# Kernel tuning notes

Measured on AMD Instinct MI355X. Metric: run time of the kernel, lower is better.

Reference implementation:

```python
import jax, jax.numpy as jnp
import numpy as np

D_MODEL = 1024
NUM_HEADS = 16
DEPTH = D_MODEL // NUM_HEADS


def setup_inputs() -> dict:
    key = jax.random.key(0)
    ks = jax.random.split(key, 9)
    B, S = 2, 2048
    s = 1.0 / np.sqrt(D_MODEL)
    return {
        "x": jax.random.normal(ks[0], (B, S, D_MODEL), dtype=jnp.float32),
        "wq": jax.random.normal(ks[1], (D_MODEL, D_MODEL), dtype=jnp.float32) * s,
        "bq": jnp.zeros((D_MODEL,), dtype=jnp.float32),
        "wk": jax.random.normal(ks[2], (D_MODEL, D_MODEL), dtype=jnp.float32) * s,
        "bk": jnp.zeros((D_MODEL,), dtype=jnp.float32),
        "wv": jax.random.normal(ks[3], (D_MODEL, D_MODEL), dtype=jnp.float32) * s,
        "bv": jnp.zeros((D_MODEL,), dtype=jnp.float32),
        "wo": jax.random.normal(ks[4], (D_MODEL, D_MODEL), dtype=jnp.float32) * s,
        "bo": jnp.zeros((D_MODEL,), dtype=jnp.float32),
    }


def _split_heads(t):
    # [B, S, D] -> [B, H, S, depth]
    B, S, _ = t.shape
    return t.reshape(B, S, NUM_HEADS, DEPTH).transpose(0, 2, 1, 3)


def reference(x, wq, bq, wk, bk, wv, bv, wo, bo):
    B, S, _ = x.shape
    q = _split_heads(x @ wq + bq)
    k = _split_heads(x @ wk + bk)
    v = _split_heads(x @ wv + bv)
    scale = 1.0 / jnp.sqrt(jnp.asarray(DEPTH, dtype=x.dtype))
    logits = jnp.einsum("bhsd,bhtd->bhst", q, k) * scale  # [B,H,S,S]
    attn = jax.nn.softmax(logits, axis=-1)
    ctx = jnp.einsum("bhst,bhtd->bhsd", attn, v)  # [B,H,S,depth]
    concat = ctx.transpose(0, 2, 1, 3).reshape(B, S, D_MODEL)
    return concat @ wo + bo
```

## Files before the change

kernel.cpp:

```cpp
#include <hip/hip_runtime.h>
#include <hip/hip_bf16.h>

typedef __bf16 bf16;
typedef __bf16 bf16x4 __attribute__((ext_vector_type(4)));
typedef __bf16 bf16x8 __attribute__((ext_vector_type(8)));
typedef float f32x4 __attribute__((ext_vector_type(4)));

typedef __attribute__((address_space(3))) void lds_void;
typedef const __attribute__((address_space(1))) void gbl_void;

#define D_MODEL 1024
#define NHEAD 16
#define DEPTH 64
#define SEQ 2048
#define BATCH 2
#define NTOK (BATCH * SEQ)

#define Q_SCALE 0.18033688f

__global__ __launch_bounds__(256) void prep(const float* __restrict__ w0,
                                            const float* __restrict__ w1,
                                            const float* __restrict__ w2,
                                            const float* __restrict__ w3,
                                            const float* __restrict__ x,
                                            bf16* __restrict__ wtb,
                                            bf16* __restrict__ xb) {
    int z = blockIdx.z;
    int tx = threadIdx.x, ty = threadIdx.y;
    if (z < 4) {
        const float* w = (z == 0) ? w0 : (z == 1) ? w1 : (z == 2) ? w2 : w3;
        bf16* d = wtb + (size_t)z * D_MODEL * D_MODEL;
        __shared__ float tile[32][33];
        int c0 = blockIdx.x * 32;
        int r0 = blockIdx.y * 32;
#pragma unroll
        for (int i = 0; i < 4; i++)
            tile[ty + i * 8][tx] = w[(size_t)(r0 + ty + i * 8) * D_MODEL + c0 + tx];
        __syncthreads();
#pragma unroll
        for (int i = 0; i < 4; i++)
            d[(size_t)(c0 + ty + i * 8) * D_MODEL + r0 + tx] = (bf16)tile[tx][ty + i * 8];
    } else {
        int t = ty * 32 + tx;
        size_t i = ((size_t)(z - 4) * 1024 + blockIdx.y * 32 + blockIdx.x) * 256 + t;
        float4 v = ((const float4*)x)[i];
        bf16x4 o = {(bf16)v.x, (bf16)v.y, (bf16)v.z, (bf16)v.w};
        *(bf16x4*)&xb[i * 4] = o;
    }
}

template <bool SWAP>
__device__ __forceinline__ void gemm_core(const bf16* __restrict__ A,
                                          const bf16* __restrict__ Bt,
                                          int row0, int col0,
                                          bf16* As, bf16* Bs, f32x4 acc[4][4]) {
    const int tid = threadIdx.x;
    const int lane = tid & 63, wave = tid >> 6;
    const int quad = lane >> 4, l16 = lane & 15;
    const int wm = (wave & 1) << 6, wn = (wave >> 1) << 6;
    const int srow = lane >> 2, selem = (lane & 3) * 8;

    for (int k0 = 0; k0 < D_MODEL; k0 += 32) {
        __syncthreads();
#pragma unroll
        for (int t = 0; t < 2; t++) {
            int m = wave * 2 + t;
            const bf16* ga = A + (size_t)(row0 + m * 16 + srow) * D_MODEL + k0 + selem;
            const bf16* gb = Bt + (size_t)(col0 + m * 16 + srow) * D_MODEL + k0 + selem;
            __builtin_amdgcn_global_load_lds((gbl_void*)ga, (lds_void*)(As + m * 512 + lane * 8), 16, 0, 0);
            __builtin_amdgcn_global_load_lds((gbl_void*)gb, (lds_void*)(Bs + m * 512 + lane * 8), 16, 0, 0);
        }
        __syncthreads();
        bf16x8 af[4], bfr[4];
#pragma unroll
        for (int i = 0; i < 4; i++)
            af[i] = *(const bf16x8*)&As[(wm + i * 16 + l16) * 32 + quad * 8];
#pragma unroll
        for (int j = 0; j < 4; j++)
            bfr[j] = *(const bf16x8*)&Bs[(wn + j * 16 + l16) * 32 + quad * 8];
#pragma unroll
        for (int i = 0; i < 4; i++)
#pragma unroll
            for (int j = 0; j < 4; j++)
                acc[i][j] = SWAP
                    ? __builtin_amdgcn_mfma_f32_16x16x32_bf16(bfr[j], af[i], acc[i][j], 0, 0, 0)
                    : __builtin_amdgcn_mfma_f32_16x16x32_bf16(af[i], bfr[j], acc[i][j], 0, 0, 0);
    }
}

__global__ __launch_bounds__(256) void qkv_gemm(const bf16* __restrict__ xb,
                                                const bf16* __restrict__ wtb,
                                                const float* __restrict__ bq,
                                                const float* __restrict__ bk,
                                                const float* __restrict__ bv,
                                                bf16* __restrict__ q,
                                                bf16* __restrict__ k,
                                                bf16* __restrict__ v) {
    __shared__ bf16 As[128 * 32];
    __shared__ bf16 Bs[128 * 32];
    int zc = blockIdx.x;
    int z = zc >> 3;
    const bf16* Bt = wtb + (size_t)z * D_MODEL * D_MODEL;
    const float* bias = (z == 0) ? bq : (z == 1) ? bk : bv;
    int row0 = blockIdx.y * 128, col0 = (zc & 7) * 128;
    f32x4 acc[4][4] = {};

    const int lane = threadIdx.x & 63, wave = threadIdx.x >> 6;
    const int quad = lane >> 4, l16 = lane & 15;
    const int wm = (wave & 1) << 6, wn = (wave >> 1) << 6;

    if (z < 2) {
        gemm_core<false>(xb, Bt, row0, col0, As, Bs, acc);
        bf16* dst = (z == 0) ? q : k;
        const float sc = (z == 0) ? Q_SCALE : 1.0f;
#pragma unroll
        for (int i = 0; i < 4; i++) {
#pragma unroll
            for (int j = 0; j < 4; j++) {
                int colg = col0 + wn + j * 16 + l16;
                int hh = colg >> 6, d = colg & 63;
                float bi = bias[colg];
                int rbase = row0 + wm + i * 16 + quad * 4;
                int b = rbase >> 11, sb = rbase & 2047;
#pragma unroll
                for (int r = 0; r < 4; r++) {
                    size_t idx = ((size_t)(b * NHEAD + hh) * SEQ + sb + r) * DEPTH + d;
                    dst[idx] = (bf16)((acc[i][j][r] + bi) * sc);
                }
            }
        }
    } else {
        gemm_core<true>(xb, Bt, row0, col0, As, Bs, acc);
#pragma unroll
        for (int i = 0; i < 4; i++) {
            int tok = row0 + wm + i * 16 + l16;
            int b = tok >> 11, sb = tok & 2047;
#pragma unroll
            for (int j = 0; j < 4; j++) {
#pragma unroll
                for (int r = 0; r < 4; r++) {
                    int f = col0 + wn + j * 16 + quad * 4 + r;
                    int hh = f >> 6, d = f & 63;
                    v[((size_t)(b * NHEAD + hh) * DEPTH + d) * SEQ + sb] =
                        (bf16)(acc[i][j][r] + bias[f]);
                }
            }
        }
    }
}

__global__ __launch_bounds__(256) void attn(const bf16* __restrict__ q,
                                            const bf16* __restrict__ k,
                                            const bf16* __restrict__ v,
                                            bf16* __restrict__ ctx) {
    __shared__ bf16 Ks[64 * 72];
    __shared__ bf16 Vs[64 * 72];
    __shared__ bf16 Ps[4][32 * 72];
    const int tid = threadIdx.x;
    const int lane = tid & 63, wave = tid >> 6;
    const int quad = lane >> 4, l16 = lane & 15;
    const int bh = blockIdx.x;
    const int q0 = blockIdx.y * 128;
    const size_t hb = (size_t)bh * SEQ * DEPTH;
    const bf16* qh = q + hb;
    const bf16* kh = k + hb;
    const bf16* vh = v + hb;

    bf16x8 bq_[2][2];
#pragma unroll
    for (int g = 0; g < 2; g++) {
        int qrow = q0 + wave * 32 + g * 16 + l16;
#pragma unroll
        for (int c = 0; c < 2; c++)
            bq_[g][c] = *(const bf16x8*)&qh[(size_t)qrow * DEPTH + c * 32 + quad * 8];
    }
    bf16* myP = &Ps[wave][0];

    bf16x8 ones;
#pragma unroll
    for (int i = 0; i < 8; i++) ones[i] = (bf16)1.0f;

    f32x4 ov[2][4] = {};
    f32x4 lacc[2] = {};

    const int srow = tid >> 2, scol = (tid & 3) << 4;
    const bf16* kg = kh + (size_t)srow * DEPTH + scol;
    const bf16* vg = vh + (size_t)srow * SEQ + scol;
    bf16* ksd = &Ks[srow * 72 + scol];
    bf16* vsd = &Vs[srow * 72 + scol];

    bf16x8 kr0 = *(const bf16x8*)kg, kr1 = *(const bf16x8*)(kg + 8);
    bf16x8 vr0 = *(const bf16x8*)vg, vr1 = *(const bf16x8*)(vg + 8);

    for (int t0 = 0; t0 < SEQ; t0 += 64) {
        __syncthreads();
        *(bf16x8*)ksd = kr0;  *(bf16x8*)(ksd + 8) = kr1;
        *(bf16x8*)vsd = vr0;  *(bf16x8*)(vsd + 8) = vr1;
        __syncthreads();
        if (t0 + 64 < SEQ) {
            const bf16* kgn = kg + (size_t)(t0 + 64) * DEPTH;
            const bf16* vgn = vg + (t0 + 64);
            kr0 = *(const bf16x8*)kgn;  kr1 = *(const bf16x8*)(kgn + 8);
            vr0 = *(const bf16x8*)vgn;  vr1 = *(const bf16x8*)(vgn + 8);
        }
        f32x4 sc[2][4] = {};
#pragma unroll
        for (int c = 0; c < 2; c++)
#pragma unroll
            for (int j = 0; j < 4; j++) {
                bf16x8 kf = *(const bf16x8*)&Ks[(j * 16 + l16) * 72 + c * 32 + quad * 8];
#pragma unroll
                for (int g = 0; g < 2; g++)
                    sc[g][j] = __builtin_amdgcn_mfma_f32_16x16x32_bf16(kf, bq_[g][c], sc[g][j], 0, 0, 0);
            }
#pragma unroll
        for (int g = 0; g < 2; g++)
#pragma unroll
            for (int j = 0; j < 4; j++) {
                bf16x4 pb = {(bf16)__builtin_amdgcn_exp2f(sc[g][j][0]),
                             (bf16)__builtin_amdgcn_exp2f(sc[g][j][1]),
                             (bf16)__builtin_amdgcn_exp2f(sc[g][j][2]),
                             (bf16)__builtin_amdgcn_exp2f(sc[g][j][3])};
                *(bf16x4*)&myP[(g * 16 + l16) * 72 + j * 16 + quad * 4] = pb;
            }
#pragma unroll
        for (int c = 0; c < 2; c++) {
            bf16x8 pf[2];
#pragma unroll
            for (int g = 0; g < 2; g++) {
                pf[g] = *(const bf16x8*)&myP[(g * 16 + l16) * 72 + c * 32 + quad * 8];
                lacc[g] = __builtin_amdgcn_mfma_f32_16x16x32_bf16(ones, pf[g], lacc[g], 0, 0, 0);
            }
#pragma unroll
            for (int t = 0; t < 4; t++) {
                bf16x8 vf = *(const bf16x8*)&Vs[(t * 16 + l16) * 72 + c * 32 + quad * 8];
#pragma unroll
                for (int g = 0; g < 2; g++)
                    ov[g][t] = __builtin_amdgcn_mfma_f32_16x16x32_bf16(vf, pf[g], ov[g][t], 0, 0, 0);
            }
        }
    }
    int b = bh >> 4, hh = bh & 15;
#pragma unroll
    for (int g = 0; g < 2; g++) {
        float inv = 1.0f / lacc[g][0];
        size_t rowb = ((size_t)(b * SEQ + q0 + wave * 32 + g * 16 + l16)) * D_MODEL + hh * 64;
#pragma unroll
        for (int t = 0; t < 4; t++) {
            bf16x4 ob = {(bf16)(ov[g][t][0] * inv), (bf16)(ov[g][t][1] * inv),
                         (bf16)(ov[g][t][2] * inv), (bf16)(ov[g][t][3] * inv)};
            *(bf16x4*)&ctx[rowb + t * 16 + quad * 4] = ob;
        }
    }
}

__global__ __launch_bounds__(256) void out_gemm(const bf16* __restrict__ ctx,
                                                const bf16* __restrict__ wot,
                                                const float* __restrict__ bo,
                                                float* __restrict__ out) {
    __shared__ bf16 As[64 * 32];
    __shared__ bf16 Bs[128 * 32];
    const int tid = threadIdx.x;
    const int lane = tid & 63, wave = tid >> 6;
    const int quad = lane >> 4, l16 = lane & 15;
    const int srow = lane >> 2, selem = (lane & 3) * 8;
    int row0 = blockIdx.y * 64, col0 = blockIdx.x * 128;
    f32x4 acc[4][2] = {};

    for (int k0 = 0; k0 < D_MODEL; k0 += 32) {
        __syncthreads();
        {
            const bf16* ga = ctx + (size_t)(row0 + wave * 16 + srow) * D_MODEL + k0 + selem;
            __builtin_amdgcn_global_load_lds((gbl_void*)ga, (lds_void*)(As + wave * 512 + lane * 8), 16, 0, 0);
        }
#pragma unroll
        for (int t = 0; t < 2; t++) {
            int m = wave * 2 + t;
            const bf16* gb = wot + (size_t)(col0 + m * 16 + srow) * D_MODEL + k0 + selem;
            __builtin_amdgcn_global_load_lds((gbl_void*)gb, (lds_void*)(Bs + m * 512 + lane * 8), 16, 0, 0);
        }
        __syncthreads();
        bf16x8 af[4], bfr[2];
#pragma unroll
        for (int i = 0; i < 4; i++)
            af[i] = *(const bf16x8*)&As[(i * 16 + l16) * 32 + quad * 8];
#pragma unroll
        for (int j = 0; j < 2; j++)
            bfr[j] = *(const bf16x8*)&Bs[(wave * 32 + j * 16 + l16) * 32 + quad * 8];
#pragma unroll
        for (int i = 0; i < 4; i++)
#pragma unroll
            for (int j = 0; j < 2; j++)
                acc[i][j] = __builtin_amdgcn_mfma_f32_16x16x32_bf16(af[i], bfr[j], acc[i][j], 0, 0, 0);
    }
#pragma unroll
    for (int i = 0; i < 4; i++)
#pragma unroll
        for (int j = 0; j < 2; j++) {
            int colg = col0 + wave * 32 + j * 16 + l16;
            float bi = bo[colg];
            int rbase = row0 + i * 16 + quad * 4;
#pragma unroll
            for (int r = 0; r < 4; r++)
                out[(size_t)(rbase + r) * D_MODEL + colg] = acc[i][j][r] + bi;
        }
}

extern "C" void kernel_launch(void* const* d_in, const int* in_sizes, int n_in,
                              void* d_out, int out_size, void* d_ws, size_t ws_size,
                              hipStream_t stream) {
    const float* x  = (const float*)d_in[0];
    const float* wq = (const float*)d_in[1];
    const float* bq = (const float*)d_in[2];
    const float* wk = (const float*)d_in[3];
    const float* bk = (const float*)d_in[4];
    const float* wv = (const float*)d_in[5];
    const float* bv = (const float*)d_in[6];
    const float* wo = (const float*)d_in[7];
    const float* bo = (const float*)d_in[8];
    float* out = (float*)d_out;

    const size_t MB = 1024 * 1024;
    char* ws = (char*)d_ws;
    bf16* xb  = (bf16*)(ws);
    bf16* wtb = (bf16*)(ws + 8 * MB);
    bf16* qb  = (bf16*)(ws + 16 * MB);
    bf16* kb  = (bf16*)(ws + 24 * MB);
    bf16* vb  = (bf16*)(ws + 32 * MB);
    bf16* ctx = (bf16*)(ws + 40 * MB);

    prep<<<dim3(32, 32, 8), dim3(32, 8), 0, stream>>>(wq, wk, wv, wo, x, wtb, xb);
    qkv_gemm<<<dim3(24, 32), 256, 0, stream>>>(xb, wtb, bq, bk, bv, qb, kb, vb);
    attn<<<dim3(BATCH * NHEAD, SEQ / 128), 256, 0, stream>>>(qb, kb, vb, ctx);
    out_gemm<<<dim3(8, 64), 256, 0, stream>>>(ctx, wtb + 3 * (size_t)D_MODEL * D_MODEL, bo, out);
}
```

Measured before the change: 206.3 us.

## Rewrite QKV GEMM with 256x256 tiles, double-buffered LDS pipeline and swizzle

The QKV projection kernel moves from 128x128 tiles with a single-buffered, sync-heavy K loop to 256x256 tiles on 512 threads. It double-buffers 64-wide K stages in LDS, interleaves global-to-LDS loads with MFMA phases under explicit vmcnt waits and barriers, uses an XOR swizzle to avoid LDS bank conflicts, remaps workgroups for L2 locality, and vectorises the V-transpose stores. The aim is to hide memory latency and raise data reuse per block. The trade-off is a launch of only 192 blocks, using 128KB of LDS, which may underfill the GPU's CUs.

```diff
diff --git a/kernel.cpp b/kernel.cpp
--- a/kernel.cpp
+++ b/kernel.cpp
@@ -49,101 +49,145 @@
     }
 }
 
-template <bool SWAP>
-__device__ __forceinline__ void gemm_core(const bf16* __restrict__ A,
-                                          const bf16* __restrict__ Bt,
-                                          int row0, int col0,
-                                          bf16* As, bf16* Bs, f32x4 acc[4][4]) {
+__global__ __launch_bounds__(512, 2) void qkv_gemm(const bf16* __restrict__ xb,
+                                                   const bf16* __restrict__ wtb,
+                                                   const float* __restrict__ bq,
+                                                   const float* __restrict__ bk,
+                                                   const float* __restrict__ bv,
+                                                   bf16* __restrict__ q,
+                                                   bf16* __restrict__ k,
+                                                   bf16* __restrict__ v) {
+    __shared__ bf16 sm[65536];
+
+    const int flat = blockIdx.x;
+    const int wg = (flat & 7) * 24 + (flat >> 3);
+    const int mt = wg & 15, nt = wg >> 4;
+    const int row0 = mt << 8;
+    const int z = nt >> 2;
+    const int nb = (nt & 3) << 8;
+
     const int tid = threadIdx.x;
     const int lane = tid & 63, wave = tid >> 6;
+    const int wm = wave >> 2, wn = wave & 3;
     const int quad = lane >> 4, l16 = lane & 15;
-    const int wm = (wave & 1) << 6, wn = (wave >> 1) << 6;
-    const int srow = lane >> 2, selem = (lane & 3) * 8;
-
-    for (int k0 = 0; k0 < D_MODEL; k0 += 32) {
-        __syncthreads();
-#pragma unroll
-        for (int t = 0; t < 2; t++) {
-            int m = wave * 2 + t;
-            const bf16* ga = A + (size_t)(row0 + m * 16 + srow) * D_MODEL + k0 + selem;
-            const bf16* gb = Bt + (size_t)(col0 + m * 16 + srow) * D_MODEL + k0 + selem;
-            __builtin_amdgcn_global_load_lds((gbl_void*)ga, (lds_void*)(As + m * 512 + lane * 8), 16, 0, 0);
-            __builtin_amdgcn_global_load_lds((gbl_void*)gb, (lds_void*)(Bs + m * 512 + lane * 8), 16, 0, 0);
-        }
-        __syncthreads();
-        bf16x8 af[4], bfr[4];
-#pragma unroll
-        for (int i = 0; i < 4; i++)
-            af[i] = *(const bf16x8*)&As[(wm + i * 16 + l16) * 32 + quad * 8];
-#pragma unroll
-        for (int j = 0; j < 4; j++)
-            bfr[j] = *(const bf16x8*)&Bs[(wn + j * 16 + l16) * 32 + quad * 8];
-#pragma unroll
-        for (int i = 0; i < 4; i++)
-#pragma unroll
-            for (int j = 0; j < 4; j++)
-                acc[i][j] = SWAP
-                    ? __builtin_amdgcn_mfma_f32_16x16x32_bf16(bfr[j], af[i], acc[i][j], 0, 0, 0)
-                    : __builtin_amdgcn_mfma_f32_16x16x32_bf16(af[i], bfr[j], acc[i][j], 0, 0, 0);
-    }
-}
-
-__global__ __launch_bounds__(256) void qkv_gemm(const bf16* __restrict__ xb,
-                                                const bf16* __restrict__ wtb,
-                                                const float* __restrict__ bq,
-                                                const float* __restrict__ bk,
-                                                const float* __restrict__ bv,
-                                                bf16* __restrict__ q,
-                                                bf16* __restrict__ k,
-                                                bf16* __restrict__ v) {
-    __shared__ bf16 As[128 * 32];
-    __shared__ bf16 Bs[128 * 32];
-    int zc = blockIdx.x;
-    int z = zc >> 3;
-    const bf16* Bt = wtb + (size_t)z * D_MODEL * D_MODEL;
+    const int kch = ((quad ^ ((l16 >> 1) & 3)) << 3);
+
+    const int srow = lane >> 2;
+    const int scg = (lane & 3) ^ ((lane >> 3) & 3);
+    const int stDst = wave * 1024 + lane * 8;
+
+    const bf16* Ag = xb + (size_t)(row0 + wave * 32 + srow) * D_MODEL + scg * 8;
+    const bf16* Bg = wtb + (size_t)z * D_MODEL * D_MODEL
+                   + (size_t)(nb + wave * 32 + srow) * D_MODEL + scg * 8;
+
+    f32x4 acc[8][4] = {};
+    bf16x8 bfr[4];
+
+#define GLL(SRC, DST) __builtin_amdgcn_global_load_lds((gbl_void*)(SRC), (lds_void*)(DST), 16, 0, 0)
+#define STG_A(T_, KQ_, BUF_) { \
+    const bf16* s_ = Ag + (T_) * 64 + (KQ_) * 32; \
+    bf16* d_ = sm + (BUF_) * 16384 + (KQ_) * 8192 + stDst; \
+    GLL(s_, d_); GLL(s_ + 16 * D_MODEL, d_ + 512); }
+#define STG_B(T_, KQ_, BUF_) { \
+    const bf16* s_ = Bg + (T_) * 64 + (KQ_) * 32; \
+    bf16* d_ = sm + 32768 + (BUF_) * 16384 + (KQ_) * 8192 + stDst; \
+    GLL(s_, d_); GLL(s_ + 16 * D_MODEL, d_ + 512); }
+#define WAIT6 { asm volatile("s_waitcnt vmcnt(6)" ::: "memory"); }
+#define NOW
+
+#define PHASE(BUF_, KQ_, MQ_, STG_STMT, WAIT_STMT) { \
+    bf16x8 af[4]; \
+    const int ab_ = (BUF_) * 16384 + (KQ_) * 8192 + (wm * 128 + (MQ_) * 64 + l16) * 32 + kch; \
+    _Pragma("unroll") \
+    for (int i_ = 0; i_ < 4; i_++) af[i_] = *(const bf16x8*)&sm[ab_ + i_ * 512]; \
+    if ((MQ_) == 0) { \
+        const int bb_ = 32768 + (BUF_) * 16384 + (KQ_) * 8192 + (wn * 64 + l16) * 32 + kch; \
+        _Pragma("unroll") \
+        for (int j_ = 0; j_ < 4; j_++) bfr[j_] = *(const bf16x8*)&sm[bb_ + j_ * 512]; \
+    } \
+    STG_STMT; \
+    WAIT_STMT; \
+    __builtin_amdgcn_sched_barrier(0); \
+    __builtin_amdgcn_s_barrier(); \
+    __builtin_amdgcn_s_setprio(1); \
+    _Pragma("unroll") \
+    for (int i_ = 0; i_ < 4; i_++) \
+        _Pragma("unroll") \
+        for (int j_ = 0; j_ < 4; j_++) \
+            acc[(MQ_) * 4 + i_][j_] = __builtin_amdgcn_mfma_f32_16x16x32_bf16( \
+                af[i_], bfr[j_], acc[(MQ_) * 4 + i_][j_], 0, 0, 0); \
+    __builtin_amdgcn_s_setprio(0); \
+    __builtin_amdgcn_sched_barrier(0); \
+    __builtin_amdgcn_s_barrier(); }
+
+    STG_B(0, 0, 0);
+    STG_A(0, 0, 0);
+    STG_B(0, 1, 0);
+    STG_A(0, 1, 0);
+    asm volatile("s_waitcnt vmcnt(4)" ::: "memory");
+    STG_B(1, 0, 1);
+    STG_A(1, 0, 1);
+    STG_B(1, 1, 1);
+    asm volatile("s_waitcnt vmcnt(6)" ::: "memory");
+    __builtin_amdgcn_sched_barrier(0);
+    __builtin_amdgcn_s_barrier();
+
+#pragma unroll 1
+    for (int it = 0; it < 8; ++it) {
+        const int t1 = 2 * it + 1;
+        const int t2 = (2 * it + 2) & 15;
+        const int t3 = (2 * it + 3) & 15;
+        PHASE(0, 0, 0, STG_A(t1, 1, 1), NOW)
+        PHASE(0, 0, 1, STG_B(t2, 0, 0), NOW)
+        PHASE(0, 1, 0, STG_A(t2, 0, 0), NOW)
+        PHASE(0, 1, 1, STG_B(t2, 1, 0), WAIT6)
+        PHASE(1, 0, 0, STG_A(t2, 1, 0), NOW)
+        PHASE(1, 0, 1, STG_B(t3, 0, 1), NOW)
+        PHASE(1, 1, 0, STG_A(t3, 0, 1), NOW)
+        PHASE(1, 1, 1, STG_B(t3, 1, 1), WAIT6)
+    }
+
+#undef PHASE
+#undef WAIT6
+#undef NOW
+#undef STG_A
+#undef STG_B
+#undef GLL
+
     const float* bias = (z == 0) ? bq : (z == 1) ? bk : bv;
-    int row0 = blockIdx.y * 128, col0 = (zc & 7) * 128;
-    f32x4 acc[4][4] = {};
-
-    const int lane = threadIdx.x & 63, wave = threadIdx.x >> 6;
-    const int quad = lane >> 4, l16 = lane & 15;
-    const int wm = (wave & 1) << 6, wn = (wave >> 1) << 6;
-
+    const int bI = row0 >> 11;
+    const int sBase = row0 & 2047;
     if (z < 2) {
-        gemm_core<false>(xb, Bt, row0, col0, As, Bs, acc);
         bf16* dst = (z == 0) ? q : k;
-        const float sc = (z == 0) ? Q_SCALE : 1.0f;
-#pragma unroll
-        for (int i = 0; i < 4; i++) {
-#pragma unroll
-            for (int j = 0; j < 4; j++) {
-                int colg = col0 + wn + j * 16 + l16;
-                int hh = colg >> 6, d = colg & 63;
-                float bi = bias[colg];
-                int rbase = row0 + wm + i * 16 + quad * 4;
-                int b = rbase >> 11, sb = rbase & 2047;
-#pragma unroll
-                for (int r = 0; r < 4; r++) {
-                    size_t idx = ((size_t)(b * NHEAD + hh) * SEQ + sb + r) * DEPTH + d;
-                    dst[idx] = (bf16)((acc[i][j][r] + bi) * sc);
-                }
+        const float scl = (z == 0) ? Q_SCALE : 1.0f;
+#pragma unroll
+        for (int j = 0; j < 4; j++) {
+            const int f = nb + wn * 64 + j * 16 + l16;
+            const float bi = bias[f];
+            const int hh = f >> 6, d = f & 63;
+            bf16* dcol = dst + ((size_t)(bI * NHEAD + hh) * SEQ) * DEPTH + d;
+#pragma unroll
+            for (int mi = 0; mi < 8; mi++) {
+                const int s0 = sBase + wm * 128 + (mi >> 2) * 64 + (mi & 3) * 16 + quad * 4;
+#pragma unroll
+                for (int r = 0; r < 4; r++)
+                    dcol[(size_t)(s0 + r) * DEPTH] = (bf16)((acc[mi][j][r] + bi) * scl);
             }
         }
     } else {
-        gemm_core<true>(xb, Bt, row0, col0, As, Bs, acc);
-#pragma unroll
-        for (int i = 0; i < 4; i++) {
-            int tok = row0 + wm + i * 16 + l16;
-            int b = tok >> 11, sb = tok & 2047;
-#pragma unroll
-            for (int j = 0; j < 4; j++) {
-#pragma unroll
-                for (int r = 0; r < 4; r++) {
-                    int f = col0 + wn + j * 16 + quad * 4 + r;
-                    int hh = f >> 6, d = f & 63;
-                    v[((size_t)(b * NHEAD + hh) * DEPTH + d) * SEQ + sb] =
-                        (bf16)(acc[i][j][r] + bias[f]);
-                }
+#pragma unroll
+        for (int j = 0; j < 4; j++) {
+            const int f = nb + wn * 64 + j * 16 + l16;
+            const float bi = bias[f];
+            const int hh = f >> 6, d = f & 63;
+            bf16* vrow = v + ((size_t)(bI * NHEAD + hh) * DEPTH + d) * SEQ;
+#pragma unroll
+            for (int mi = 0; mi < 8; mi++) {
+                const int s0 = sBase + wm * 128 + (mi >> 2) * 64 + (mi & 3) * 16 + quad * 4;
+                f32x4 a = acc[mi][j];
+                bf16x4 ob = {(bf16)(a[0] + bi), (bf16)(a[1] + bi),
+                             (bf16)(a[2] + bi), (bf16)(a[3] + bi)};
+                *(bf16x4*)&vrow[s0] = ob;
             }
         }
     }
@@ -330,7 +374,7 @@
     bf16* ctx = (bf16*)(ws + 40 * MB);
 
     prep<<<dim3(32, 32, 8), dim3(32, 8), 0, stream>>>(wq, wk, wv, wo, x, wtb, xb);
-    qkv_gemm<<<dim3(24, 32), 256, 0, stream>>>(xb, wtb, bq, bk, bv, qb, kb, vb);
+    qkv_gemm<<<dim3(192), dim3(512), 0, stream>>>(xb, wtb, bq, bk, bv, qb, kb, vb);
     attn<<<dim3(BATCH * NHEAD, SEQ / 128), 256, 0, stream>>>(qb, kb, vb, ctx);
     out_gemm<<<dim3(8, 64), 256, 0, stream>>>(ctx, wtb + 3 * (size_t)D_MODEL * D_MODEL, bo, out);
 }
```

New measurement: 193.2 us. 6.4% less time.
